# Performance work log

Measured on AMD Instinct MI355X. Metric: run time of the kernel, lower is better.

## Reference

```python
import jax, jax.numpy as jnp
import numpy as np

D_STATE = 8
DT_RANK = 16
D_CONV = 4


def layernorm(x, w, b, eps=1e-5):
    mu = jnp.mean(x, axis=-1, keepdims=True)
    var = jnp.var(x, axis=-1, keepdims=True)
    return (x - mu) * jax.lax.rsqrt(var + eps) * w + b


def silu(x):
    return x * jax.nn.sigmoid(x)


def dwconv_causal(x, w, b):
    # x: [B,L,D], w: [D,K] depthwise causal conv (mamba conv1d, padding=K-1 then truncate)
    K = w.shape[1]
    xp = jnp.pad(x, ((0, 0), (K - 1, 0), (0, 0)))
    y = jax.lax.conv_general_dilated(
        xp, w.T[:, None, :], (1,), 'VALID',
        dimension_numbers=('NWC', 'WIO', 'NWC'),
        feature_group_count=w.shape[0])
    return y + b


def selective_scan(u, dt, A, Bm, Cm, Dp):
    # u, dt: [b,l,d]; A: [d,n]; Bm, Cm: [b,l,n]; Dp: [d]
    def step(h, inp):
        dt_t, B_t, C_t, u_t = inp           # [b,d],[b,n],[b,n],[b,d]
        dA = jnp.exp(dt_t[..., None] * A)   # [b,d,n]
        h = dA * h + dt_t[..., None] * B_t[:, None, :] * u_t[..., None]
        y = jnp.einsum('bdn,bn->bd', h, C_t)
        return h, y
    b, l, d = u.shape
    h0 = jnp.zeros((b, d, A.shape[1]), u.dtype)
    xs = (dt.transpose(1, 0, 2), Bm.transpose(1, 0, 2),
          Cm.transpose(1, 0, 2), u.transpose(1, 0, 2))
    _, ys = jax.lax.scan(step, h0, xs)
    return ys.transpose(1, 0, 2) + u * Dp


def scan_dir(x, xe, cw, cb, cew, ceb, xpw, dtw, dtb, A_log, Dp):
    # one scan direction: u from x (input0 path), dt/B/C from xe (extra_emb path)
    xc = silu(dwconv_causal(x, cw, cb))
    ec = silu(dwconv_causal(xe, cew, ceb))
    dbl = ec @ xpw.T                                   # [b,l,dt_rank+2n]
    dtr = dbl[..., :DT_RANK]
    Bm = dbl[..., DT_RANK:DT_RANK + D_STATE]
    Cm = dbl[..., DT_RANK + D_STATE:]
    dt = jax.nn.softplus(dtr @ dtw.T + dtb)
    A = -jnp.exp(A_log)
    return selective_scan(xc, dt, A, Bm, Cm, Dp)


def forward(input0, input1, norm0_w, norm0_b, norm1_w, norm1_b,
            in_proj_w, in_proj_extra_w,
            convx_w, convx_b, conve_w, conve_b,
            convx_w_r, convx_b_r, conve_w_r, conve_b_r,
            xproj_w, xproj_w_r, dtproj_w, dtproj_b, dtproj_w_r, dtproj_b_r,
            A_log, A_log_r, Dp, Dp_r, outnorm_w, outnorm_b, outproj_w):
    skip = input0
    h0 = layernorm(input0, norm0_w, norm0_b)
    h1 = layernorm(input1, norm1_w, norm1_b)
    xz = h0 @ in_proj_w.T                     # [b,l,2d]
    d = in_proj_w.shape[0] // 2
    x, z = xz[..., :d], xz[..., d:]
    xe = h1 @ in_proj_extra_w.T               # [b,l,d]
    # forward-direction scan
    y_f = scan_dir(x, xe, convx_w, convx_b, conve_w, conve_b,
                   xproj_w, dtproj_w, dtproj_b, A_log, Dp)
    # backward-direction scan (flip sequence, scan, flip back)
    xr, xer = jnp.flip(x, 1), jnp.flip(xe, 1)
    y_b = scan_dir(xr, xer, convx_w_r, convx_b_r, conve_w_r, conve_b_r,
                   xproj_w_r, dtproj_w_r, dtproj_b_r, A_log_r, Dp_r)
    y = (y_f + jnp.flip(y_b, 1)) * 0.5        # if_devide_out=True
    y = layernorm(y, outnorm_w, outnorm_b)    # use_norm=True
    y = y * silu(z)
    out = y @ outproj_w.T
    return out + skip


def setup_inputs() -> dict:
    key = jax.random.key(0)
    B, H, W, dim = 2, 128, 128, 256
    L, d, n, dtr, K = H * W, dim, D_STATE, DT_RANK, D_CONV
    ks = jax.random.split(key, 24)
    s = 0.02
    inp = {
        'input0': jax.random.normal(ks[0], (B, L, dim), jnp.float32),
        'input1': jax.random.normal(ks[1], (B, L, dim), jnp.float32),
        'norm0_w': jnp.ones((dim,), jnp.float32),
        'norm0_b': jnp.zeros((dim,), jnp.float32),
        'norm1_w': jnp.ones((dim,), jnp.float32),
        'norm1_b': jnp.zeros((dim,), jnp.float32),
        'in_proj_w': jax.random.normal(ks[2], (2 * d, dim), jnp.float32) * s,
        'in_proj_extra_w': jax.random.normal(ks[3], (d, dim), jnp.float32) * s,
        'convx_w': jax.random.normal(ks[4], (d, K), jnp.float32) * 0.2,
        'convx_b': jnp.zeros((d,), jnp.float32),
        'conve_w': jax.random.normal(ks[5], (d, K), jnp.float32) * 0.2,
        'conve_b': jnp.zeros((d,), jnp.float32),
        'convx_w_r': jax.random.normal(ks[6], (d, K), jnp.float32) * 0.2,
        'convx_b_r': jnp.zeros((d,), jnp.float32),
        'conve_w_r': jax.random.normal(ks[7], (d, K), jnp.float32) * 0.2,
        'conve_b_r': jnp.zeros((d,), jnp.float32),
        'xproj_w': jax.random.normal(ks[8], (dtr + 2 * n, d), jnp.float32) * s,
        'xproj_w_r': jax.random.normal(ks[9], (dtr + 2 * n, d), jnp.float32) * s,
        'dtproj_w': jax.random.normal(ks[10], (d, dtr), jnp.float32) * 0.1,
        'dtproj_b': jax.random.uniform(ks[11], (d,), jnp.float32, -4.0, -2.0),
        'dtproj_w_r': jax.random.normal(ks[12], (d, dtr), jnp.float32) * 0.1,
        'dtproj_b_r': jax.random.uniform(ks[13], (d,), jnp.float32, -4.0, -2.0),
        'A_log': jnp.tile(jnp.log(jnp.arange(1, n + 1, dtype=jnp.float32)), (d, 1)),
        'A_log_r': jnp.tile(jnp.log(jnp.arange(1, n + 1, dtype=jnp.float32)), (d, 1)),
        'Dp': jnp.ones((d,), jnp.float32),
        'Dp_r': jnp.ones((d,), jnp.float32),
        'outnorm_w': jnp.ones((d,), jnp.float32),
        'outnorm_b': jnp.zeros((d,), jnp.float32),
        'outproj_w': jax.random.normal(ks[14], (dim, d), jnp.float32) * s,
    }
    return inp


def reference(input0, input1, norm0_w, norm0_b, norm1_w, norm1_b,
              in_proj_w, in_proj_extra_w,
              convx_w, convx_b, conve_w, conve_b,
              convx_w_r, convx_b_r, conve_w_r, conve_b_r,
              xproj_w, xproj_w_r, dtproj_w, dtproj_b, dtproj_w_r, dtproj_b_r,
              A_log, A_log_r, Dp, Dp_r, outnorm_w, outnorm_b, outproj_w):
    return forward(input0, input1, norm0_w, norm0_b, norm1_w, norm1_b,
                   in_proj_w, in_proj_extra_w,
                   convx_w, convx_b, conve_w, conve_b,
                   convx_w_r, convx_b_r, conve_w_r, conve_b_r,
                   xproj_w, xproj_w_r, dtproj_w, dtproj_b, dtproj_w_r, dtproj_b_r,
                   A_log, A_log_r, Dp, Dp_r, outnorm_w, outnorm_b, outproj_w)
```

## Files before the change

### kernel.cpp

```cpp
#include <hip/hip_runtime.h>
#include <math.h>

#define L_SEQ 16384
#define DIM 256
#define NST 8
#define RNK 16
#define S_TOT 32768
#define NCH 512
#define CLH 32

typedef __attribute__((ext_vector_type(8))) short bf16x8;
typedef __attribute__((ext_vector_type(4))) float f32x4;

__device__ __forceinline__ float bf2f(unsigned short u) {
  union { unsigned int i; float f; } v; v.i = ((unsigned int)u) << 16; return v.f;
}
__device__ __forceinline__ unsigned short f2bf(float x) {
  union { float f; unsigned int i; } v; v.f = x;
  unsigned int r = v.i + 0x7fffu + ((v.i >> 16) & 1u);
  return (unsigned short)(r >> 16);
}
__device__ __forceinline__ float rcpf(float x) {
  return __builtin_amdgcn_rcpf(x);
}
// ... 34 lines not shown
  out.x = f2bf((v.x - mean) * rstd * wv.x + bv.x);
  out.y = f2bf((v.y - mean) * rstd * wv.y + bv.y);
  out.z = f2bf((v.z - mean) * rstd * wv.z + bv.z);
  out.w = f2bf((v.w - mean) * rstd * wv.w + bv.w);
  *(ushort4*)&h[(size_t)row * DIM + lane * 4] = out;
}

template <int BF16C, int ADDIN>
__global__ __launch_bounds__(256) void gemm64(
    const unsigned short* __restrict__ A, int lda,
    const unsigned short* __restrict__ Wb,
    void* __restrict__ Cv, const float* __restrict__ addp, int Nn) {
  __shared__ unsigned short As[64 * 256];
  __shared__ unsigned short Ws[64 * 256];
  int tid = threadIdx.x;
  int n0 = blockIdx.x * 64, m0 = blockIdx.y * 64;
  for (int i = 0; i < 8; ++i) {
    int f8 = tid + i * 256;
    int r = f8 >> 5, c8 = (f8 & 31) * 8;
    int sc = c8 ^ ((r & 7) << 3);
    *(uint4*)&As[r * 256 + sc] = *(const uint4*)&A[(size_t)(m0 + r) * lda + c8];
    *(uint4*)&Ws[r * 256 + sc] = *(const uint4*)&Wb[(size_t)(n0 + r) * 256 + c8];
  }
  __syncthreads();
  int wid = tid >> 6, lane = tid & 63;
  int wm = wid >> 1, wn = wid & 1;
  int l15 = lane & 15, lk = (lane >> 4) * 8;
  f32x4 acc[2][2] = {};
  for (int ks = 0; ks < 8; ++ks) {
    int kcol = ks * 32 + lk;
    bf16x8 af[2], bf_[2];
    for (int mf = 0; mf < 2; ++mf) {
      int row = wm * 32 + mf * 16 + l15;
      af[mf] = *(const bf16x8*)&As[row * 256 + (kcol ^ ((row & 7) << 3))];
    }
    for (int nf = 0; nf < 2; ++nf) {
      int row = wn * 32 + nf * 16 + l15;
      bf_[nf] = *(const bf16x8*)&Ws[row * 256 + (kcol ^ ((row & 7) << 3))];
    }
    for (int mf = 0; mf < 2; ++mf)
      for (int nf = 0; nf < 2; ++nf)
        acc[mf][nf] = __builtin_amdgcn_mfma_f32_16x16x32_bf16(
            af[mf], bf_[nf], acc[mf][nf], 0, 0, 0);
  }
  for (int mf = 0; mf < 2; ++mf)
    for (int nf = 0; nf < 2; ++nf) {
      int row = m0 + wm * 32 + mf * 16 + (lane >> 4) * 4;
      int col = n0 + wn * 32 + nf * 16 + l15;
      for (int v = 0; v < 4; ++v) {
        size_t off = (size_t)(row + v) * Nn + col;
        float val = acc[mf][nf][v];
        if (ADDIN) val += addp[off];
        if (BF16C) ((unsigned short*)Cv)[off] = f2bf(val);
        else       ((float*)Cv)[off] = val;
      }
    }
}

__global__ __launch_bounds__(256) void gemm_in2(
    const unsigned short* __restrict__ h0, const unsigned short* __restrict__ h1,
    const unsigned short* __restrict__ wb_in, const unsigned short* __restrict__ wb_ex,
    unsigned short* __restrict__ xzOut, unsigned short* __restrict__ xeOut) {
  __shared__ unsigned short As[64 * 256];
  __shared__ unsigned short Ws[64 * 256];
  int tid = threadIdx.x;
  bool isX = blockIdx.x < 512;
  const unsigned short* A = isX ? h0 : h1;
  const unsigned short* Wb = isX ? wb_in : wb_ex;
  unsigned short* Cv = isX ? xzOut : xeOut;
  int Nn = isX ? 512 : 256;
  int NT = isX ? 8 : 4;
  int m0 = (isX ? (int)blockIdx.x : (int)blockIdx.x - 512) * 64;
  for (int i = 0; i < 8; ++i) {
    int f8 = tid + i * 256;
    int r = f8 >> 5, c8 = (f8 & 31) * 8;
    int sc = c8 ^ ((r & 7) << 3);
    *(uint4*)&As[r * 256 + sc] = *(const uint4*)&A[(size_t)(m0 + r) * 256 + c8];
  }
  int wid = tid >> 6, lane = tid & 63;
  int wm = wid >> 1, wn = wid & 1;
  int l15 = lane & 15, lk = (lane >> 4) * 8;
  for (int nt = 0; nt < NT; ++nt) {
    int n0 = nt * 64;
    for (int i = 0; i < 8; ++i) {
      int f8 = tid + i * 256;
      int r = f8 >> 5, c8 = (f8 & 31) * 8;
      int sc = c8 ^ ((r & 7) << 3);
      *(uint4*)&Ws[r * 256 + sc] = *(const uint4*)&Wb[(size_t)(n0 + r) * 256 + c8];
    }
    __syncthreads();
    f32x4 acc[2][2] = {};
    for (int ks = 0; ks < 8; ++ks) {
      int kcol = ks * 32 + lk;
      bf16x8 af[2], bf_[2];
      for (int mf = 0; mf < 2; ++mf) {
        int row = wm * 32 + mf * 16 + l15;
        af[mf] = *(const bf16x8*)&As[row * 256 + (kcol ^ ((row & 7) << 3))];
      }
      for (int nf = 0; nf < 2; ++nf) {
        int row = wn * 32 + nf * 16 + l15;
        bf_[nf] = *(const bf16x8*)&Ws[row * 256 + (kcol ^ ((row & 7) << 3))];
      }
      for (int mf = 0; mf < 2; ++mf)
        for (int nf = 0; nf < 2; ++nf)
          acc[mf][nf] = __builtin_amdgcn_mfma_f32_16x16x32_bf16(
              af[mf], bf_[nf], acc[mf][nf], 0, 0, 0);
    }
    for (int mf = 0; mf < 2; ++mf)
      for (int nf = 0; nf < 2; ++nf) {
        int row = m0 + wm * 32 + mf * 16 + (lane >> 4) * 4;
        int col = n0 + wn * 32 + nf * 16 + l15;
        for (int v = 0; v < 4; ++v) {
          size_t off = (size_t)(row + v) * Nn + col;
          Cv[off] = f2bf(acc[mf][nf][v]);
        }
      }
    __syncthreads();
  }
}

__global__ __launch_bounds__(256) void gemm_out3(
    const unsigned short* __restrict__ ycomb,
    const unsigned short* __restrict__ ybu,
    const unsigned short* __restrict__ xz,
    const float* __restrict__ onw, const float* __restrict__ onb,
    const unsigned short* __restrict__ Wb,
    float* __restrict__ outp, const float* __restrict__ addp) {
  __shared__ unsigned short As[64 * 256];
  __shared__ unsigned short Ws[64 * 256];
  int tid = threadIdx.x;
  int m0 = (int)blockIdx.x * 64;
  for (int i = 0; i < 8; ++i) {
    int f8 = tid + i * 256;
    int r = f8 >> 5, c8 = (f8 & 31) * 8;
    int sc = c8 ^ ((r & 7) << 3);
    int m = m0 + r;
    int b = m >> 14, l = m & (L_SEQ - 1);
    const unsigned short* pf = &ycomb[(size_t)m * DIM + c8];
    const unsigned short* pb =
        &ybu[((size_t)S_TOT + ((size_t)b << 14) + (L_SEQ - 1 - l)) * DIM + c8];
    ushort4 f0 = *(const ushort4*)pf, f1 = *(const ushort4*)(pf + 4);
    ushort4 b0 = *(const ushort4*)pb, b1 = *(const ushort4*)(pb + 4);
    float v[8];
    v[0] = 0.5f * (bf2f(f0.x) + bf2f(b0.x));
    v[1] = 0.5f * (bf2f(f0.y) + bf2f(b0.y));
    v[2] = 0.5f * (bf2f(f0.z) + bf2f(b0.z));
    v[3] = 0.5f * (bf2f(f0.w) + bf2f(b0.w));
    v[4] = 0.5f * (bf2f(f1.x) + bf2f(b1.x));
    v[5] = 0.5f * (bf2f(f1.y) + bf2f(b1.y));
    v[6] = 0.5f * (bf2f(f1.z) + bf2f(b1.z));
    v[7] = 0.5f * (bf2f(f1.w) + bf2f(b1.w));
    float s = 0.f, s2 = 0.f;
    for (int j = 0; j < 8; ++j) { s += v[j]; s2 += v[j] * v[j]; }
    for (int off = 16; off; off >>= 1) {
      s += __shfl_xor(s, off);
      s2 += __shfl_xor(s2, off);
    }
    float mean = s * (1.0f / DIM);
    float var = s2 * (1.0f / DIM) - mean * mean;
    float rstd = rsqrtf(var + 1e-5f);
    const unsigned short* pz = &xz[(size_t)m * 512 + 256 + c8];
    ushort4 z0 = *(const ushort4*)pz, z1 = *(const ushort4*)(pz + 4);
    float zf[8] = {bf2f(z0.x), bf2f(z0.y), bf2f(z0.z), bf2f(z0.w),
                   bf2f(z1.x), bf2f(z1.y), bf2f(z1.z), bf2f(z1.w)};
    float4 w0v = *(const float4*)&onw[c8];
    float4 w1v = *(const float4*)&onw[c8 + 4];
    float4 bb0 = *(const float4*)&onb[c8];
    float4 bb1 = *(const float4*)&onb[c8 + 4];
    float wv[8] = {w0v.x, w0v.y, w0v.z, w0v.w, w1v.x, w1v.y, w1v.z, w1v.w};
    float bv[8] = {bb0.x, bb0.y, bb0.z, bb0.w, bb1.x, bb1.y, bb1.z, bb1.w};
    unsigned int o[4];
    for (int jj = 0; jj < 4; ++jj) {
      int j0 = jj * 2, j1 = jj * 2 + 1;
      float ln0 = (v[j0] - mean) * rstd * wv[j0] + bv[j0];
      float ln1 = (v[j1] - mean) * rstd * wv[j1] + bv[j1];
      float g0 = ln0 * (zf[j0] * rcpf(1.f + __expf(-zf[j0])));
      float g1 = ln1 * (zf[j1] * rcpf(1.f + __expf(-zf[j1])));
      o[jj] = (unsigned int)f2bf(g0) | ((unsigned int)f2bf(g1) << 16);
    }
    uint4 pk; pk.x = o[0]; pk.y = o[1]; pk.z = o[2]; pk.w = o[3];
    *(uint4*)&As[r * 256 + sc] = pk;
  }
  int wid = tid >> 6, lane = tid & 63;
  int wm = wid >> 1, wn = wid & 1;
  int l15 = lane & 15, lk = (lane >> 4) * 8;
  for (int nt = 0; nt < 4; ++nt) {
    int n0 = nt * 64;
    for (int i = 0; i < 8; ++i) {
      int f8 = tid + i * 256;
      int r = f8 >> 5, c8 = (f8 & 31) * 8;
      int sc = c8 ^ ((r & 7) << 3);
      *(uint4*)&Ws[r * 256 + sc] = *(const uint4*)&Wb[(size_t)(n0 + r) * 256 + c8];
    }
    __syncthreads();
    f32x4 acc[2][2] = {};
    for (int ks = 0; ks < 8; ++ks) {
      int kcol = ks * 32 + lk;
      bf16x8 af[2], bf_[2];
      for (int mf = 0; mf < 2; ++mf) {
        int row = wm * 32 + mf * 16 + l15;
        af[mf] = *(const bf16x8*)&As[row * 256 + (kcol ^ ((row & 7) << 3))];
      }
      for (int nf = 0; nf < 2; ++nf) {
        int row = wn * 32 + nf * 16 + l15;
        bf_[nf] = *(const bf16x8*)&Ws[row * 256 + (kcol ^ ((row & 7) << 3))];
      }
      for (int mf = 0; mf < 2; ++mf)
        for (int nf = 0; nf < 2; ++nf)
          acc[mf][nf] = __builtin_amdgcn_mfma_f32_16x16x32_bf16(
              af[mf], bf_[nf], acc[mf][nf], 0, 0, 0);
    }
    for (int mf = 0; mf < 2; ++mf)
      for (int nf = 0; nf < 2; ++nf) {
        int row = m0 + wm * 32 + mf * 16 + (lane >> 4) * 4;
        int col = n0 + wn * 32 + nf * 16 + l15;
        for (int v = 0; v < 4; ++v) {
          size_t off = (size_t)(row + v) * 256 + col;
          outp[off] = acc[mf][nf][v] + addp[off];
        }
      }
    __syncthreads();
  }
}

__global__ __launch_bounds__(256) void xproj_mfma(
    const unsigned short* __restrict__ xe,
    const float* __restrict__ conve_w, const float* __restrict__ conve_b,
    const float* __restrict__ conve_w_r, const float* __restrict__ conve_b_r,
    const float* __restrict__ xproj_w, const float* __restrict__ xproj_w_r,
    unsigned short* __restrict__ dbl2) {
  __shared__ unsigned short ecS[64 * 256];
  __shared__ unsigned short xwS[32 * 256];
  int chunk = blockIdx.x;
  int dir = blockIdx.y;
  int b = chunk >> 8;
  int t0 = (chunk & 255) * 64;
  int tid = threadIdx.x;
  const float* cw = dir ? conve_w_r : conve_w;
  const float* cb = dir ? conve_b_r : conve_b;
  const float* xw = dir ? xproj_w_r : xproj_w;

  for (int i = tid; i < 32 * 256; i += 256) {
    int o = i >> 8, dd = i & 255;
    xwS[o * 256 + (((dd & ~7) ^ ((o & 7) << 3)) | (dd & 7))] = f2bf(xw[i]);
  }

  {
    int c = tid;
    float w0 = cw[c * 4 + 0], w1 = cw[c * 4 + 1], w2 = cw[c * 4 + 2],
          w3 = cw[c * 4 + 3], bias = cb[c];
    size_t bL = (size_t)b * L_SEQ;
    auto loadx = [&](int t) -> float {
      if (t < 0) return 0.f;
      int src = dir ? (L_SEQ - 1 - t) : t;
      return bf2f(xe[(bL + src) * DIM + c]);
    };
    float xm3 = loadx(t0 - 3), xm2 = loadx(t0 - 2), xm1 = loadx(t0 - 1);
    const unsigned short* xp =
        &xe[(bL + (dir ? (L_SEQ - 1 - t0) : t0)) * DIM + c];
    int xstep = dir ? -DIM : DIM;
    int cbase = c & ~7, clow = c & 7;
    for (int t4 = 0; t4 < 64; t4 += 4) {
      float xin4[4];
      for (int j = 0; j < 4; ++j) xin4[j] = bf2f(xp[(ptrdiff_t)j * xstep]);
      xp += (ptrdiff_t)4 * xstep;
      for (int j = 0; j < 4; ++j) {
        int tl = t4 + j;
        float xin = xin4[j];
        float pre = w0 * xm3 + w1 * xm2 + w2 * xm1 + w3 * xin + bias;
        float u = pre * rcpf(1.f + __expf(-pre));
        xm3 = xm2; xm2 = xm1; xm1 = xin;
        ecS[tl * 256 + ((cbase ^ ((tl & 7) << 3)) | clow)] = f2bf(u);
      }
    }
  }
  __syncthreads();

  int wid = tid >> 6, lane = tid & 63;
  int l15 = lane & 15, lk = (lane >> 4) * 8;
  f32x4 acc[2] = {};
  for (int kk = 0; kk < 8; ++kk) {
    int kcol = kk * 32 + lk;
    int row = wid * 16 + l15;
    bf16x8 af = *(const bf16x8*)&ecS[row * 256 + (kcol ^ ((row & 7) << 3))];
    for (int ni = 0; ni < 2; ++ni) {
      int o = ni * 16 + l15;
      bf16x8 bfr = *(const bf16x8*)&xwS[o * 256 + (kcol ^ ((o & 7) << 3))];
      acc[ni] = __builtin_amdgcn_mfma_f32_16x16x32_bf16(af, bfr, acc[ni], 0, 0, 0);
    }
  }
  size_t mbase = (size_t)dir * S_TOT + (size_t)chunk * 64;
  int rloc = wid * 16 + (lane >> 4) * 4;
  for (int ni = 0; ni < 2; ++ni) {
    int o = ni * 16 + l15;
    for (int v = 0; v < 4; ++v)
      dbl2[(mbase + rloc + v) * 32 + o] = f2bf(acc[ni][v]);
  }
}

__global__ __launch_bounds__(256) void dtu_compute(
    const unsigned short* __restrict__ dbl2,
    const float* __restrict__ dtw, const float* __restrict__ dtw_r,
    const float* __restrict__ dtb, const float* __restrict__ dtb_r,
    unsigned short* __restrict__ dt_arr,
    const unsigned short* __restrict__ xz,
    const float* __restrict__ convx_w, const float* __restrict__ convx_b,
    const float* __restrict__ convx_w_r, const float* __restrict__ convx_b_r,
    unsigned short* __restrict__ u_arr) {
  __shared__ unsigned short dtwS[256 * 32];
  __shared__ unsigned short dtrS[64 * 32];
  __shared__ unsigned short outS[64 * 256];
  int tid = threadIdx.x;
  if (blockIdx.x < 1024) {
    int m0 = blockIdx.x * 64;
    int dir = (blockIdx.x >= 512) ? 1 : 0;
    const float* dw = dir ? dtw_r : dtw;
    const float* db = dir ? dtb_r : dtb;
    {
      uint4 z; z.x = 0; z.y = 0; z.z = 0; z.w = 0;
      for (int i = tid; i < 1280; i += 256) {
        if (i < 1024) ((uint4*)dtwS)[i] = z;
        else          ((uint4*)dtrS)[i - 1024] = z;
      }
    }
    __syncthreads();
    for (int it = 0; it < 4; ++it) {
      int idx = tid + it * 256;
      int c = idx >> 2, k4 = idx & 3;
      float4 v = *(const float4*)&dw[c * 16 + k4 * 4];
      uint2 pk;
      pk.x = (unsigned int)f2bf(v.x) | ((unsigned int)f2bf(v.y) << 16);
      pk.y = (unsigned int)f2bf(v.z) | ((unsigned int)f2bf(v.w) << 16);
      int byte = c * 64 + (((k4 >> 1) ^ (c & 3)) << 4) + ((k4 & 1) << 3);
      *(uint2*)((char*)dtwS + byte) = pk;
    }
    {
      int r = tid >> 2, k4 = tid & 3;
      uint2 pk = *(const uint2*)&dbl2[(size_t)(m0 + r) * 32 + k4 * 4];
      int byte = r * 64 + (((k4 >> 1) ^ (r & 3)) << 4) + ((k4 & 1) << 3);
      *(uint2*)((char*)dtrS + byte) = pk;
    }
    __syncthreads();
    int wid = tid >> 6, lane = tid & 63;
    int l15 = lane & 15, lkc = lane >> 4;
    bf16x8 af[4];
    for (int mi = 0; mi < 4; ++mi) {
      int r = mi * 16 + l15;
      af[mi] = *(const bf16x8*)((char*)dtrS + r * 64 + ((lkc ^ (r & 3)) << 4));
    }
    f32x4 acc[4][4] = {};
    for (int ni = 0; ni < 4; ++ni) {
      int c = (wid * 4 + ni) * 16 + l15;
      bf16x8 bfr = *(const bf16x8*)((char*)dtwS + c * 64 + ((lkc ^ (c & 3)) << 4));
      for (int mi = 0; mi < 4; ++mi)
        acc[mi][ni] = __builtin_amdgcn_mfma_f32_16x16x32_bf16(
            af[mi], bfr, acc[mi][ni], 0, 0, 0);
    }
    for (int ni = 0; ni < 4; ++ni) {
      int c = (wid * 4 + ni) * 16 + l15;
      float bias_ = db[c];
      int cb_ = c & ~7, cl_ = c & 7;
      for (int mi = 0; mi < 4; ++mi) {
        int rb = mi * 16 + (lane >> 4) * 4;
        for (int v = 0; v < 4; ++v) {
          int r = rb + v;
          float xdt = acc[mi][ni][v] + bias_;
          float dtv = (xdt > 15.f) ? xdt : __logf(1.f + __expf(xdt));
          outS[r * 256 + ((cb_ ^ ((r & 7) << 3)) | cl_)] = f2bf(dtv);
        }
      }
    }
    __syncthreads();
    for (int it = 0; it < 8; ++it) {
      int i = tid + it * 256;
      int r = i >> 5, cg = (i & 31) * 8;
      uint4 val = *(const uint4*)&outS[r * 256 + (cg ^ ((r & 7) << 3))];
      *(uint4*)&dt_arr[(size_t)(m0 + r) * 256 + cg] = val;
    }
  } else {
    int chunk = blockIdx.x - 1024;
    int b = chunk >> 9;
    int t0 = (chunk & 511) * 32;
    int c = tid;
    float w0 = convx_w[c * 4 + 0], w1 = convx_w[c * 4 + 1],
          w2 = convx_w[c * 4 + 2], w3 = convx_w[c * 4 + 3], bias = convx_b[c];
    float w0r = convx_w_r[c * 4 + 0], w1r = convx_w_r[c * 4 + 1],
          w2r = convx_w_r[c * 4 + 2], w3r = convx_w_r[c * 4 + 3],
          biasr = convx_b_r[c];
    size_t bL = (size_t)b * L_SEQ;
    auto ld = [&](int t) -> float {
      if (t < 0 || t >= L_SEQ) return 0.f;
      return bf2f(xz[(bL + t) * 512 + c]);
    };
    float x3 = ld(t0 - 3), x2 = ld(t0 - 2), x1 = ld(t0 - 1);
    unsigned short* op0 = &u_arr[(bL + t0) * DIM + c];
    unsigned short* op1 =
        &u_arr[((size_t)S_TOT + bL + (L_SEQ - 1 - t0)) * DIM + c];
    for (int tg = 0; tg < 36; tg += 4) {
      float xin4[4];
      for (int j = 0; j < 4; ++j) xin4[j] = ld(t0 + tg + j);
      for (int j = 0; j < 4; ++j) {
        int tl = tg + j;
        float xin = xin4[j];
        if (tl < 32) {
          float pre = w0 * x3 + w1 * x2 + w2 * x1 + w3 * xin + bias;
          op0[(size_t)tl * DIM] = f2bf(pre * rcpf(1.f + __expf(-pre)));
        }
        if (tl >= 3 && tl < 35) {
          float prer = w0r * xin + w1r * x1 + w2r * x2 + w3r * x3 + biasr;
          int s = tl - 3;
          *(op1 - (ptrdiff_t)s * DIM) = f2bf(prer * rcpf(1.f + __expf(-prer)));
        }
        x3 = x2; x2 = x1; x1 = xin;
      }
    }
  }
}

#define DA8(FASTA)                                                    \
  float dA[NST];                                                      \
  if (FASTA) {                                                        \
    float e1 = __expf(-dtv);                                          \
    dA[0] = e1;                                                       \
    for (int n = 1; n < NST; ++n) dA[n] = dA[n - 1] * e1;             \
  } else {                                                            \
    for (int n = 0; n < NST; ++n) dA[n] = __expf(dtv * Ar[n]);        \
  }

template <int USE_UDT>
__global__ __launch_bounds__(256) void scan_pass1(
    const unsigned short* __restrict__ xz, const unsigned short* __restrict__ dbl2,
    const unsigned short* __restrict__ u_arr,
    const unsigned short* __restrict__ dt_arr,
    const float* __restrict__ convx_w, const float* __restrict__ convx_b,
    const float* __restrict__ convx_w_r, const float* __restrict__ convx_b_r,
    const float* __restrict__ dtproj_w, const float* __restrict__ dtproj_b,
    const float* __restrict__ dtproj_w_r, const float* __restrict__ dtproj_b_r,
    const float* __restrict__ A_log, const float* __restrict__ A_log_r,
    float* __restrict__ Pc, float* __restrict__ Qc) {
  int chunk = blockIdx.x, b = blockIdx.y, dir = blockIdx.z;
  int d = threadIdx.x;
  const float* al = dir ? A_log_r : A_log;
  float w0 = 0.f, w1 = 0.f, w2 = 0.f, w3 = 0.f, bias = 0.f, dbias = 0.f;
  float dwreg[RNK];
  if (!USE_UDT) {
    const float* cw = dir ? convx_w_r : convx_w;
    const float* cb = dir ? convx_b_r : convx_b;
    const float* dw = dir ? dtproj_w_r : dtproj_w;
    const float* dbp = dir ? dtproj_b_r : dtproj_b;
    w0 = cw[d * 4 + 0]; w1 = cw[d * 4 + 1]; w2 = cw[d * 4 + 2];
    w3 = cw[d * 4 + 3]; bias = cb[d]; dbias = dbp[d];
    for (int r = 0; r < RNK; ++r) dwreg[r] = dw[d * RNK + r];
  }
  float Ar[NST];
  bool fa = true;
  for (int n = 0; n < NST; ++n) {
    Ar[n] = -__expf(al[d * NST + n]);
    fa = fa && (fabsf(Ar[n] + (float)(n + 1)) < 1e-4f * (float)(n + 1));
  }
  bool fastA = (__ballot(fa) == ~0ULL);

  __shared__ float dblS[CLH][32];
  int t0 = chunk * CLH;
  size_t dtbase = (size_t)dir * S_TOT + (size_t)b * L_SEQ;
  if (USE_UDT) {
    int i = d;
    dblS[i >> 3][i & 7] =
        bf2f(dbl2[(dtbase + t0 + (i >> 3)) * 32 + 16 + (i & 7)]);
  } else {
    for (int i = d; i < CLH * 32; i += 256)
      dblS[i >> 5][i & 31] = bf2f(dbl2[(dtbase + t0) * 32 + i]);
  }
  __syncthreads();
  auto loadx = [&](int t) -> float {
    if (t < 0) return 0.f;
    int srct = dir ? (L_SEQ - 1 - t) : t;
    return bf2f(xz[((size_t)b * L_SEQ + srct) * 512 + d]);
  };
  float xm3 = 0.f, xm2 = 0.f, xm1 = 0.f;
  if (!USE_UDT) { xm3 = loadx(t0 - 3); xm2 = loadx(t0 - 2); xm1 = loadx(t0 - 1); }
  const unsigned short* up = &u_arr[(dtbase + t0) * DIM + d];
  const unsigned short* dtp = &dt_arr[(dtbase + t0) * DIM + d];
  float Q[NST];
  for (int n = 0; n < NST; ++n) Q[n] = 0.f;
  float sdt = 0.f;
  const int BOFF = USE_UDT ? 0 : 16;

#define P1_GRP(FASTA)                                                      \
  for (int t8 = 0; t8 < CLH; t8 += 8) {                                    \
    float uu[8], dd[8];                                                    \
    for (int j = 0; j < 8; ++j) {                                          \
      uu[j] = bf2f(up[(size_t)j * DIM]);                                   \
      dd[j] = bf2f(dtp[(size_t)j * DIM]);                                  \
    }                                                                      \
    up += 8 * DIM; dtp += 8 * DIM;                                         \
    for (int j = 0; j < 8; ++j) {                                          \
      const float* row = dblS[t8 + j];                                     \
      float u = uu[j], dtv = dd[j];                                        \
      float du = dtv * u;                                                  \
      sdt += dtv;                                                          \
      DA8(FASTA)                                                           \
      float4 B0 = *(const float4*)(row);                                   \
      float4 B1 = *(const float4*)(row + 4);                               \
      Q[0] = dA[0] * Q[0] + du * B0.x; Q[1] = dA[1] * Q[1] + du * B0.y;    \
      Q[2] = dA[2] * Q[2] + du * B0.z; Q[3] = dA[3] * Q[3] + du * B0.w;    \
      Q[4] = dA[4] * Q[4] + du * B1.x; Q[5] = dA[5] * Q[5] + du * B1.y;    \
      Q[6] = dA[6] * Q[6] + du * B1.z; Q[7] = dA[7] * Q[7] + du * B1.w;    \
    }                                                                      \
  }

#define P1_STEP(FASTA)                                                     \
  {                                                                        \
    const float* row = dblS[tl];                                           \
    float u, dtv;                                                          \
    {                                                                      \
      float xin = loadx(t0 + tl);                                          \
      float pre = w0 * xm3 + w1 * xm2 + w2 * xm1 + w3 * xin + bias;        \
      u = pre * rcpf(1.f + __expf(-pre));                                  \
      xm3 = xm2; xm2 = xm1; xm1 = xin;                                     \
      float4 q0 = *(const float4*)(row);                                   \
      float4 q1 = *(const float4*)(row + 4);                               \
      float4 q2 = *(const float4*)(row + 8);                               \
      float4 q3 = *(const float4*)(row + 12);                              \
      float xdt = dbias + q0.x * dwreg[0] + q0.y * dwreg[1] +              \
                  q0.z * dwreg[2] + q0.w * dwreg[3] + q1.x * dwreg[4] +    \
                  q1.y * dwreg[5] + q1.z * dwreg[6] + q1.w * dwreg[7] +    \
                  q2.x * dwreg[8] + q2.y * dwreg[9] + q2.z * dwreg[10] +   \
                  q2.w * dwreg[11] + q3.x * dwreg[12] + q3.y * dwreg[13] + \
                  q3.z * dwreg[14] + q3.w * dwreg[15];                     \
      dtv = (xdt > 15.f) ? xdt : __logf(1.f + __expf(xdt));                \
    }                                                                      \
    float du = dtv * u;                                                    \
    sdt += dtv;                                                            \
    DA8(FASTA)                                                             \
    float4 B0 = *(const float4*)(row + BOFF);                              \
    float4 B1 = *(const float4*)(row + BOFF + 4);                          \
    Q[0] = dA[0] * Q[0] + du * B0.x; Q[1] = dA[1] * Q[1] + du * B0.y;      \
    Q[2] = dA[2] * Q[2] + du * B0.z; Q[3] = dA[3] * Q[3] + du * B0.w;      \
    Q[4] = dA[4] * Q[4] + du * B1.x; Q[5] = dA[5] * Q[5] + du * B1.y;      \
    Q[6] = dA[6] * Q[6] + du * B1.z; Q[7] = dA[7] * Q[7] + du * B1.w;      \
  }

  if (USE_UDT) {
    if (fastA) { P1_GRP(1) } else { P1_GRP(0) }
  } else {
    if (fastA) {
      for (int tl = 0; tl < CLH; ++tl) P1_STEP(1)
    } else {
      for (int tl = 0; tl < CLH; ++tl) P1_STEP(0)
    }
  }
#undef P1_STEP
#undef P1_GRP

  float P[NST];
  if (fastA) {
    float E = __expf(-sdt);
    P[0] = E;
    for (int n = 1; n < NST; ++n) P[n] = P[n - 1] * E;
  } else {
    for (int n = 0; n < NST; ++n) P[n] = __expf(Ar[n] * sdt);
  }
  size_t obase = ((((size_t)(dir * 2 + b)) * NCH + chunk) * DIM + d) * NST;
  for (int n = 0; n < NST; ++n) { Pc[obase + n] = P[n]; Qc[obase + n] = Q[n]; }
}

__global__ __launch_bounds__(256) void scan_mid(
    float* __restrict__ Pc, const float* __restrict__ Qc) {
  int idx = blockIdx.x * 256 + threadIdx.x;
  int dn = idx & 2047;
  int db_ = idx >> 11;
  size_t base = (size_t)db_ * NCH * 2048 + dn;
  float h = 0.f;
  for (int c0 = 0; c0 < NCH; c0 += 8) {
    size_t off = base + (size_t)c0 * 2048;
    float P[8], Q[8];
#pragma unroll
    for (int j = 0; j < 8; ++j) {
      P[j] = Pc[off + (size_t)j * 2048];
      Q[j] = Qc[off + (size_t)j * 2048];
    }
#pragma unroll
    for (int j = 0; j < 8; ++j) {
      Pc[off + (size_t)j * 2048] = h;
      h = P[j] * h + Q[j];
    }
  }
}

template <int MODE>
__global__ __launch_bounds__(256) void scan_pass2(
    const unsigned short* __restrict__ xz, const unsigned short* __restrict__ dbl2,
    unsigned short* __restrict__ u_arr,
    const unsigned short* __restrict__ dt_arr,
    const float* __restrict__ convx_w, const float* __restrict__ convx_b,
    const float* __restrict__ convx_w_r, const float* __restrict__ convx_b_r,
    const float* __restrict__ dtproj_w, const float* __restrict__ dtproj_b,
    const float* __restrict__ dtproj_w_r, const float* __restrict__ dtproj_b_r,
    const float* __restrict__ A_log, const float* __restrict__ A_log_r,
    const float* __restrict__ Dp, const float* __restrict__ Dp_r,
    const float* __restrict__ Hinit, unsigned short* __restrict__ ycomb,
    int dirParam) {
  int chunk = blockIdx.x, b = blockIdx.y;
  int dir = MODE ? blockIdx.z : dirParam;
  int d = threadIdx.x;
  const float* al = dir ? A_log_r : A_log;
  float Dv = (dir ? Dp_r : Dp)[d];
  float w0 = 0.f, w1 = 0.f, w2 = 0.f, w3 = 0.f, bias = 0.f, dbias = 0.f;
  float dwreg[RNK];
  if (!MODE) {
    const float* cw = dir ? convx_w_r : convx_w;
    const float* cb = dir ? convx_b_r : convx_b;
    const float* dw = dir ? dtproj_w_r : dtproj_w;
    const float* dbp = dir ? dtproj_b_r : dtproj_b;
    w0 = cw[d * 4 + 0]; w1 = cw[d * 4 + 1]; w2 = cw[d * 4 + 2];
    w3 = cw[d * 4 + 3]; bias = cb[d];
    dbias = dbp[d];
    for (int r = 0; r < RNK; ++r) dwreg[r] = dw[d * RNK + r];
  }
  float Ar[NST];
  bool fa = true;
  for (int n = 0; n < NST; ++n) {
    Ar[n] = -__expf(al[d * NST + n]);
    fa = fa && (fabsf(Ar[n] + (float)(n + 1)) < 1e-4f * (float)(n + 1));
  }
  bool fastA = (__ballot(fa) == ~0ULL);

  __shared__ float dblS[CLH][32];
  int t0 = chunk * CLH;
  size_t dtbase = (size_t)dir * S_TOT + (size_t)b * L_SEQ;
  if (MODE) {
    for (int i = d; i < CLH * 16; i += 256)
      dblS[i >> 4][i & 15] =
          bf2f(dbl2[(dtbase + t0 + (i >> 4)) * 32 + 16 + (i & 15)]);
  } else {
    for (int i = d; i < CLH * 32; i += 256)
      dblS[i >> 5][i & 31] = bf2f(dbl2[(dtbase + t0) * 32 + i]);
  }
  __syncthreads();
  auto loadx = [&](int t) -> float {
    if (t < 0) return 0.f;
    int srct = dir ? (L_SEQ - 1 - t) : t;
    return bf2f(xz[((size_t)b * L_SEQ + srct) * 512 + d]);
  };
  float xm3 = 0.f, xm2 = 0.f, xm1 = 0.f;
  if (!MODE) { xm3 = loadx(t0 - 3); xm2 = loadx(t0 - 2); xm1 = loadx(t0 - 1); }
  float h[NST];
  size_t hbase = ((((size_t)(dir * 2 + b)) * NCH + chunk) * DIM + d) * NST;
  for (int n = 0; n < NST; ++n) h[n] = Hinit[hbase + n];
  unsigned short* up = &u_arr[(dtbase + t0) * DIM + d];
  const unsigned short* dtp = &dt_arr[(dtbase + t0) * DIM + d];
  unsigned short* yc = &ycomb[((size_t)b * L_SEQ + t0) * DIM + d];

#define P2_GRP(FASTA)                                                      \
  for (int t8 = 0; t8 < CLH; t8 += 8) {                                    \
    float uu[8], dd[8];                                                    \
    for (int j = 0; j < 8; ++j) {                                          \
      uu[j] = bf2f(up[(size_t)j * DIM]);                                   \
      dd[j] = bf2f(dtp[(size_t)j * DIM]);                                  \
    }                                                                      \
    for (int j = 0; j < 8; ++j) {                                          \
      const float* row = dblS[t8 + j];                                     \
      float u = uu[j], dtv = dd[j];                                        \
      float du = dtv * u;                                                  \
      DA8(FASTA)                                                           \
      float4 B0 = *(const float4*)(row);                                   \
      float4 B1 = *(const float4*)(row + 4);                               \
      float4 C0 = *(const float4*)(row + 8);                               \
      float4 C1 = *(const float4*)(row + 12);                              \
      h[0] = dA[0] * h[0] + du * B0.x; h[1] = dA[1] * h[1] + du * B0.y;    \
      h[2] = dA[2] * h[2] + du * B0.z; h[3] = dA[3] * h[3] + du * B0.w;    \
      h[4] = dA[4] * h[4] + du * B1.x; h[5] = dA[5] * h[5] + du * B1.y;    \
      h[6] = dA[6] * h[6] + du * B1.z; h[7] = dA[7] * h[7] + du * B1.w;    \
      float y = C0.x * h[0] + C0.y * h[1] + C0.z * h[2] + C0.w * h[3] +    \
                C1.x * h[4] + C1.y * h[5] + C1.z * h[6] + C1.w * h[7] +    \
                u * Dv;                                                    \
      if (dir == 0) yc[(size_t)j * DIM] = f2bf(y);                         \
      else          up[(size_t)j * DIM] = f2bf(y);                         \
    }                                                                      \
    up += 8 * DIM; dtp += 8 * DIM; yc += 8 * DIM;                          \
  }

#define P2_STEP(FASTA)                                                     \
  {                                                                        \
    int t = t0 + tl;                                                       \
    const float* row = dblS[tl];                                           \
    float u, dtv;                                                          \
    {                                                                      \
      float xin = loadx(t);                                                \
      float pre = w0 * xm3 + w1 * xm2 + w2 * xm1 + w3 * xin + bias;        \
      u = pre * rcpf(1.f + __expf(-pre));                                  \
      xm3 = xm2; xm2 = xm1; xm1 = xin;                                     \
      float4 q0 = *(const float4*)(row);                                   \
      float4 q1 = *(const float4*)(row + 4);                               \
      float4 q2 = *(const float4*)(row + 8);                               \
      float4 q3 = *(const float4*)(row + 12);                              \
      float xdt = dbias + q0.x * dwreg[0] + q0.y * dwreg[1] +              \
                  q0.z * dwreg[2] + q0.w * dwreg[3] + q1.x * dwreg[4] +    \
                  q1.y * dwreg[5] + q1.z * dwreg[6] + q1.w * dwreg[7] +    \
                  q2.x * dwreg[8] + q2.y * dwreg[9] + q2.z * dwreg[10] +   \
                  q2.w * dwreg[11] + q3.x * dwreg[12] + q3.y * dwreg[13] + \
                  q3.z * dwreg[14] + q3.w * dwreg[15];                     \
      dtv = (xdt > 15.f) ? xdt : __logf(1.f + __expf(xdt));                \
    }                                                                      \
    float du = dtv * u;                                                    \
    DA8(FASTA)                                                             \
    float4 B0 = *(const float4*)(row + 16);                                \
    float4 B1 = *(const float4*)(row + 20);                                \
    float4 C0 = *(const float4*)(row + 24);                                \
    float4 C1 = *(const float4*)(row + 28);                                \
    h[0] = dA[0] * h[0] + du * B0.x; h[1] = dA[1] * h[1] + du * B0.y;      \
    h[2] = dA[2] * h[2] + du * B0.z; h[3] = dA[3] * h[3] + du * B0.w;      \
    h[4] = dA[4] * h[4] + du * B1.x; h[5] = dA[5] * h[5] + du * B1.y;      \
    h[6] = dA[6] * h[6] + du * B1.z; h[7] = dA[7] * h[7] + du * B1.w;      \
    float y = C0.x * h[0] + C0.y * h[1] + C0.z * h[2] + C0.w * h[3] +      \
              C1.x * h[4] + C1.y * h[5] + C1.z * h[6] + C1.w * h[7] +      \
              u * Dv;                                                      \
    if (dir == 0) {                                                        \
      ycomb[((size_t)b * L_SEQ + t) * DIM + d] = f2bf(y);                  \
    } else {                                                               \
      size_t o = ((size_t)b * L_SEQ + (L_SEQ - 1 - t)) * DIM + d;          \
      float prev = bf2f(ycomb[o]);                                         \
      ycomb[o] = f2bf(0.5f * (prev + y));                                  \
    }                                                                      \
  }

  if (MODE) {
    if (fastA) { P2_GRP(1) } else { P2_GRP(0) }
  } else {
    if (fastA) {
      for (int tl = 0; tl < CLH; ++tl) P2_STEP(1)
    } else {
      for (int tl = 0; tl < CLH; ++tl) P2_STEP(0)
    }
  }
#undef P2_STEP
#undef P2_GRP
}

__global__ __launch_bounds__(256) void combine_ln(
    const unsigned short* __restrict__ ycomb,
    unsigned short* __restrict__ xz,
    const float* __restrict__ onw, const float* __restrict__ onb) {
  int m = blockIdx.x * 4 + (threadIdx.x >> 6);
  int lane = threadIdx.x & 63;
  ushort4 y4 = *(const ushort4*)&ycomb[(size_t)m * DIM + lane * 4];
  float v0 = bf2f(y4.x), v1 = bf2f(y4.y), v2 = bf2f(y4.z), v3 = bf2f(y4.w);
  float s = v0 + v1 + v2 + v3;
  float s2 = v0 * v0 + v1 * v1 + v2 * v2 + v3 * v3;
  for (int off = 32; off; off >>= 1) {
    s += __shfl_xor(s, off);
    s2 += __shfl_xor(s2, off);
  }
  float mean = s * (1.0f / DIM);
  float var = s2 * (1.0f / DIM) - mean * mean;
  float rstd = rsqrtf(var + 1e-5f);
  ushort4 z4 = *(const ushort4*)&xz[(size_t)m * 512 + 256 + lane * 4];
  float zf[4] = {bf2f(z4.x), bf2f(z4.y), bf2f(z4.z), bf2f(z4.w)};
  float vf[4] = {v0, v1, v2, v3};
  ushort4 out;
  unsigned short* op = (unsigned short*)&out;
  for (int j = 0; j < 4; ++j) {
    int c = lane * 4 + j;
    float ln = (vf[j] - mean) * rstd * onw[c] + onb[c];
    op[j] = f2bf(ln * (zf[j] * rcpf(1.f + __expf(-zf[j]))));
  }
  *(ushort4*)&xz[(size_t)m * 512 + lane * 4] = out;
}

extern "C" void kernel_launch(void* const* d_in, const int* in_sizes, int n_in,
                              void* d_out, int out_size, void* d_ws, size_t ws_size,
                              hipStream_t stream) {
  const float* input0 = (const float*)d_in[0];
  const float* input1 = (const float*)d_in[1];
  const float* norm0_w = (const float*)d_in[2];
  const float* norm0_b = (const float*)d_in[3];
  const float* norm1_w = (const float*)d_in[4];
  const float* norm1_b = (const float*)d_in[5];
  const float* in_proj_w = (const float*)d_in[6];
  const float* in_proj_extra_w = (const float*)d_in[7];
  const float* convx_w = (const float*)d_in[8];
  const float* convx_b = (const float*)d_in[9];
  const float* conve_w = (const float*)d_in[10];
  const float* conve_b = (const float*)d_in[11];
  const float* convx_w_r = (const float*)d_in[12];
  const float* convx_b_r = (const float*)d_in[13];
  const float* conve_w_r = (const float*)d_in[14];
  const float* conve_b_r = (const float*)d_in[15];
  const float* xproj_w = (const float*)d_in[16];
  const float* xproj_w_r = (const float*)d_in[17];
  const float* dtproj_w = (const float*)d_in[18];
  const float* dtproj_b = (const float*)d_in[19];
  const float* dtproj_w_r = (const float*)d_in[20];
  const float* dtproj_b_r = (const float*)d_in[21];
  const float* A_log = (const float*)d_in[22];
  const float* A_log_r = (const float*)d_in[23];
  const float* Dp = (const float*)d_in[24];
  const float* Dp_r = (const float*)d_in[25];
  const float* outnorm_w = (const float*)d_in[26];
  const float* outnorm_b = (const float*)d_in[27];
  const float* outproj_w = (const float*)d_in[28];

  char* w = (char*)d_ws;
  unsigned short* xz    = (unsigned short*)(w + 0);
  unsigned short* h0    = (unsigned short*)(w + 33554432);
  unsigned short* ycomb = (unsigned short*)(w + 33554432);
  float* Qc   = (float*)(w + 33554432);
  unsigned short* xe    = (unsigned short*)(w + 50331648);
  float* Pc   = (float*)(w + 50331648);
  unsigned short* dbl2 = (unsigned short*)(w + 67108864);
  unsigned short* wb = (unsigned short*)(w + 75497472);
  unsigned short* wb_in  = wb;
  unsigned short* wb_ex  = wb + 131072;
  unsigned short* wb_out = wb + 196608;
  unsigned short* u_arr  = (unsigned short*)(w + 76021760);
  unsigned short* dt_arr = (unsigned short*)(w + 109576192);
  const bool big = ws_size >= 76021760ULL + 67108864ULL;
  unsigned short* h1 = big ? u_arr : xz;

  ln_norm<<<dim3(S_TOT / 4, 2), 256, 0, stream>>>(
      input0, input1, norm0_w, norm0_b, norm1_w, norm1_b, h0, h1,
      in_proj_w, in_proj_extra_w, outproj_w, wb);
  if (big) {
    gemm_in2<<<dim3(1024), 256, 0, stream>>>(h0, h1, wb_in, wb_ex, xz, xe);
  } else {
    gemm64<1, 0><<<dim3(4, 512), 256, 0, stream>>>(h1, DIM, wb_ex, xe, nullptr, 256);
    gemm64<1, 0><<<dim3(8, 512), 256, 0, stream>>>(h0, DIM, wb_in, xz, nullptr, 512);
  }
  xproj_mfma<<<dim3(512, 2), 256, 0, stream>>>(
      xe, conve_w, conve_b, conve_w_r, conve_b_r, xproj_w, xproj_w_r, dbl2);
  if (big) {
    dtu_compute<<<dim3(2048), 256, 0, stream>>>(
        dbl2, dtproj_w, dtproj_w_r, dtproj_b, dtproj_b_r, dt_arr,
        xz, convx_w, convx_b, convx_w_r, convx_b_r, u_arr);
    scan_pass1<1><<<dim3(NCH, 2, 2), 256, 0, stream>>>(
        xz, dbl2, u_arr, dt_arr, convx_w, convx_b, convx_w_r, convx_b_r,
        dtproj_w, dtproj_b, dtproj_w_r, dtproj_b_r, A_log, A_log_r, Pc, Qc);
  } else {
    scan_pass1<0><<<dim3(NCH, 2, 2), 256, 0, stream>>>(
        xz, dbl2, u_arr, dt_arr, convx_w, convx_b, convx_w_r, convx_b_r,
        dtproj_w, dtproj_b, dtproj_w_r, dtproj_b_r, A_log, A_log_r, Pc, Qc);
  }
  scan_mid<<<dim3(32), 256, 0, stream>>>(Pc, Qc);
  if (big) {
    scan_pass2<1><<<dim3(NCH, 2, 2), 256, 0, stream>>>(
        xz, dbl2, u_arr, dt_arr, convx_w, convx_b, convx_w_r, convx_b_r,
        dtproj_w, dtproj_b, dtproj_w_r, dtproj_b_r, A_log, A_log_r,
        Dp, Dp_r, Pc, ycomb, 0);
    gemm_out3<<<dim3(512), 256, 0, stream>>>(
        ycomb, u_arr, xz, outnorm_w, outnorm_b, wb_out, (float*)d_out, input0);
  } else {
    for (int dir = 0; dir < 2; ++dir)
      scan_pass2<0><<<dim3(NCH, 2), 256, 0, stream>>>(
          xz, dbl2, u_arr, dt_arr, convx_w, convx_b, convx_w_r, convx_b_r,
          dtproj_w, dtproj_b, dtproj_w_r, dtproj_b_r, A_log, A_log_r,
          Dp, Dp_r, Pc, ycomb, dir);
    combine_ln<<<dim3(S_TOT / 4), 256, 0, stream>>>(ycomb, xz, outnorm_w, outnorm_b);
    gemm64<0, 1><<<dim3(4, 512), 256, 0, stream>>>(
        xz, 512, wb_out, d_out, input0, 256);
  }
}
```

Baseline: 194.7 us.

## Fuse x-path causal conv and SiLU into scan passes instead of materializing u

The depthwise causal conv plus SiLU that produced u is no longer run in separate blocks of dtu_compute. Both scan passes now read xz directly and recompute u on the fly from a rolling 3-tap window. This removes the u_arr write and its later reads in exchange for recomputing exp/rcp in both passes and reading the wider-strided xz rows. dtu_compute shrinks to the dt projection blocks only.

```diff
diff --git a/kernel.cpp b/kernel.cpp
--- a/kernel.cpp
+++ b/kernel.cpp
@@ -360,118 +360,75 @@
     const unsigned short* __restrict__ dbl2,
     const float* __restrict__ dtw, const float* __restrict__ dtw_r,
     const float* __restrict__ dtb, const float* __restrict__ dtb_r,
-    unsigned short* __restrict__ dt_arr,
-    const unsigned short* __restrict__ xz,
-    const float* __restrict__ convx_w, const float* __restrict__ convx_b,
-    const float* __restrict__ convx_w_r, const float* __restrict__ convx_b_r,
-    unsigned short* __restrict__ u_arr) {
+    unsigned short* __restrict__ dt_arr) {
   __shared__ unsigned short dtwS[256 * 32];
   __shared__ unsigned short dtrS[64 * 32];
   __shared__ unsigned short outS[64 * 256];
   int tid = threadIdx.x;
-  if (blockIdx.x < 1024) {
-    int m0 = blockIdx.x * 64;
-    int dir = (blockIdx.x >= 512) ? 1 : 0;
-    const float* dw = dir ? dtw_r : dtw;
-    const float* db = dir ? dtb_r : dtb;
-    {
-      uint4 z; z.x = 0; z.y = 0; z.z = 0; z.w = 0;
-      for (int i = tid; i < 1280; i += 256) {
-        if (i < 1024) ((uint4*)dtwS)[i] = z;
-        else          ((uint4*)dtrS)[i - 1024] = z;
+  int m0 = blockIdx.x * 64;
+  int dir = (blockIdx.x >= 512) ? 1 : 0;
+  const float* dw = dir ? dtw_r : dtw;
+  const float* db = dir ? dtb_r : dtb;
+  {
+    uint4 z; z.x = 0; z.y = 0; z.z = 0; z.w = 0;
+    for (int i = tid; i < 1280; i += 256) {
+      if (i < 1024) ((uint4*)dtwS)[i] = z;
+      else          ((uint4*)dtrS)[i - 1024] = z;
+    }
+  }
+  __syncthreads();
+  for (int it = 0; it < 4; ++it) {
+    int idx = tid + it * 256;
+    int c = idx >> 2, k4 = idx & 3;
+    float4 v = *(const float4*)&dw[c * 16 + k4 * 4];
+    uint2 pk;
+    pk.x = (unsigned int)f2bf(v.x) | ((unsigned int)f2bf(v.y) << 16);
+    pk.y = (unsigned int)f2bf(v.z) | ((unsigned int)f2bf(v.w) << 16);
+    int byte = c * 64 + (((k4 >> 1) ^ (c & 3)) << 4) + ((k4 & 1) << 3);
+    *(uint2*)((char*)dtwS + byte) = pk;
+  }
+  {
+    int r = tid >> 2, k4 = tid & 3;
+    uint2 pk = *(const uint2*)&dbl2[(size_t)(m0 + r) * 32 + k4 * 4];
+    int byte = r * 64 + (((k4 >> 1) ^ (r & 3)) << 4) + ((k4 & 1) << 3);
+    *(uint2*)((char*)dtrS + byte) = pk;
+  }
+  __syncthreads();
+  int wid = tid >> 6, lane = tid & 63;
+  int l15 = lane & 15, lkc = lane >> 4;
+  bf16x8 af[4];
+  for (int mi = 0; mi < 4; ++mi) {
+    int r = mi * 16 + l15;
+    af[mi] = *(const bf16x8*)((char*)dtrS + r * 64 + ((lkc ^ (r & 3)) << 4));
+  }
+  f32x4 acc[4][4] = {};
+  for (int ni = 0; ni < 4; ++ni) {
+    int c = (wid * 4 + ni) * 16 + l15;
+    bf16x8 bfr = *(const bf16x8*)((char*)dtwS + c * 64 + ((lkc ^ (c & 3)) << 4));
+    for (int mi = 0; mi < 4; ++mi)
+      acc[mi][ni] = __builtin_amdgcn_mfma_f32_16x16x32_bf16(
+          af[mi], bfr, acc[mi][ni], 0, 0, 0);
+  }
+  for (int ni = 0; ni < 4; ++ni) {
+    int c = (wid * 4 + ni) * 16 + l15;
+    float bias_ = db[c];
+    int cb_ = c & ~7, cl_ = c & 7;
+    for (int mi = 0; mi < 4; ++mi) {
+      int rb = mi * 16 + (lane >> 4) * 4;
+      for (int v = 0; v < 4; ++v) {
+        int r = rb + v;
+        float xdt = acc[mi][ni][v] + bias_;
+        float dtv = (xdt > 15.f) ? xdt : __logf(1.f + __expf(xdt));
+        outS[r * 256 + ((cb_ ^ ((r & 7) << 3)) | cl_)] = f2bf(dtv);
       }
     }
-    __syncthreads();
-    for (int it = 0; it < 4; ++it) {
-      int idx = tid + it * 256;
-      int c = idx >> 2, k4 = idx & 3;
-      float4 v = *(const float4*)&dw[c * 16 + k4 * 4];
-      uint2 pk;
-      pk.x = (unsigned int)f2bf(v.x) | ((unsigned int)f2bf(v.y) << 16);
-      pk.y = (unsigned int)f2bf(v.z) | ((unsigned int)f2bf(v.w) << 16);
-      int byte = c * 64 + (((k4 >> 1) ^ (c & 3)) << 4) + ((k4 & 1) << 3);
-      *(uint2*)((char*)dtwS + byte) = pk;
-    }
-    {
-      int r = tid >> 2, k4 = tid & 3;
-      uint2 pk = *(const uint2*)&dbl2[(size_t)(m0 + r) * 32 + k4 * 4];
-      int byte = r * 64 + (((k4 >> 1) ^ (r & 3)) << 4) + ((k4 & 1) << 3);
-      *(uint2*)((char*)dtrS + byte) = pk;
-    }
-    __syncthreads();
-    int wid = tid >> 6, lane = tid & 63;
-    int l15 = lane & 15, lkc = lane >> 4;
-    bf16x8 af[4];
-    for (int mi = 0; mi < 4; ++mi) {
-      int r = mi * 16 + l15;
-      af[mi] = *(const bf16x8*)((char*)dtrS + r * 64 + ((lkc ^ (r & 3)) << 4));
-    }
-    f32x4 acc[4][4] = {};
-    for (int ni = 0; ni < 4; ++ni) {
-      int c = (wid * 4 + ni) * 16 + l15;
-      bf16x8 bfr = *(const bf16x8*)((char*)dtwS + c * 64 + ((lkc ^ (c & 3)) << 4));
-      for (int mi = 0; mi < 4; ++mi)
-        acc[mi][ni] = __builtin_amdgcn_mfma_f32_16x16x32_bf16(
-            af[mi], bfr, acc[mi][ni], 0, 0, 0);
-    }
-    for (int ni = 0; ni < 4; ++ni) {
-      int c = (wid * 4 + ni) * 16 + l15;
-      float bias_ = db[c];
-      int cb_ = c & ~7, cl_ = c & 7;
-      for (int mi = 0; mi < 4; ++mi) {
-        int rb = mi * 16 + (lane >> 4) * 4;
-        for (int v = 0; v < 4; ++v) {
-          int r = rb + v;
-          float xdt = acc[mi][ni][v] + bias_;
-          float dtv = (xdt > 15.f) ? xdt : __logf(1.f + __expf(xdt));
-          outS[r * 256 + ((cb_ ^ ((r & 7) << 3)) | cl_)] = f2bf(dtv);
-        }
-      }
-    }
-    __syncthreads();
-    for (int it = 0; it < 8; ++it) {
-      int i = tid + it * 256;
-      int r = i >> 5, cg = (i & 31) * 8;
-      uint4 val = *(const uint4*)&outS[r * 256 + (cg ^ ((r & 7) << 3))];
-      *(uint4*)&dt_arr[(size_t)(m0 + r) * 256 + cg] = val;
-    }
-  } else {
-    int chunk = blockIdx.x - 1024;
-    int b = chunk >> 9;
-    int t0 = (chunk & 511) * 32;
-    int c = tid;
-    float w0 = convx_w[c * 4 + 0], w1 = convx_w[c * 4 + 1],
-          w2 = convx_w[c * 4 + 2], w3 = convx_w[c * 4 + 3], bias = convx_b[c];
-    float w0r = convx_w_r[c * 4 + 0], w1r = convx_w_r[c * 4 + 1],
-          w2r = convx_w_r[c * 4 + 2], w3r = convx_w_r[c * 4 + 3],
-          biasr = convx_b_r[c];
-    size_t bL = (size_t)b * L_SEQ;
-    auto ld = [&](int t) -> float {
-      if (t < 0 || t >= L_SEQ) return 0.f;
-      return bf2f(xz[(bL + t) * 512 + c]);
-    };
-    float x3 = ld(t0 - 3), x2 = ld(t0 - 2), x1 = ld(t0 - 1);
-    unsigned short* op0 = &u_arr[(bL + t0) * DIM + c];
-    unsigned short* op1 =
-        &u_arr[((size_t)S_TOT + bL + (L_SEQ - 1 - t0)) * DIM + c];
-    for (int tg = 0; tg < 36; tg += 4) {
-      float xin4[4];
-      for (int j = 0; j < 4; ++j) xin4[j] = ld(t0 + tg + j);
-      for (int j = 0; j < 4; ++j) {
-        int tl = tg + j;
-        float xin = xin4[j];
-        if (tl < 32) {
-          float pre = w0 * x3 + w1 * x2 + w2 * x1 + w3 * xin + bias;
-          op0[(size_t)tl * DIM] = f2bf(pre * rcpf(1.f + __expf(-pre)));
-        }
-        if (tl >= 3 && tl < 35) {
-          float prer = w0r * xin + w1r * x1 + w2r * x2 + w3r * x3 + biasr;
-          int s = tl - 3;
-          *(op1 - (ptrdiff_t)s * DIM) = f2bf(prer * rcpf(1.f + __expf(-prer)));
-        }
-        x3 = x2; x2 = x1; x1 = xin;
-      }
-    }
+  }
+  __syncthreads();
+  for (int it = 0; it < 8; ++it) {
+    int i = tid + it * 256;
+    int r = i >> 5, cg = (i & 31) * 8;
+    uint4 val = *(const uint4*)&outS[r * 256 + (cg ^ ((r & 7) << 3))];
+    *(uint4*)&dt_arr[(size_t)(m0 + r) * 256 + cg] = val;
   }
 }
 
@@ -499,15 +456,16 @@
   int chunk = blockIdx.x, b = blockIdx.y, dir = blockIdx.z;
   int d = threadIdx.x;
   const float* al = dir ? A_log_r : A_log;
-  float w0 = 0.f, w1 = 0.f, w2 = 0.f, w3 = 0.f, bias = 0.f, dbias = 0.f;
+  const float* cw = dir ? convx_w_r : convx_w;
+  const float* cb = dir ? convx_b_r : convx_b;
+  float w0 = cw[d * 4 + 0], w1 = cw[d * 4 + 1], w2 = cw[d * 4 + 2],
+        w3 = cw[d * 4 + 3], bias = cb[d];
+  float dbias = 0.f;
   float dwreg[RNK];
   if (!USE_UDT) {
-    const float* cw = dir ? convx_w_r : convx_w;
-    const float* cb = dir ? convx_b_r : convx_b;
     const float* dw = dir ? dtproj_w_r : dtproj_w;
     const float* dbp = dir ? dtproj_b_r : dtproj_b;
-    w0 = cw[d * 4 + 0]; w1 = cw[d * 4 + 1]; w2 = cw[d * 4 + 2];
-    w3 = cw[d * 4 + 3]; bias = cb[d]; dbias = dbp[d];
+    dbias = dbp[d];
     for (int r = 0; r < RNK; ++r) dwreg[r] = dw[d * RNK + r];
   }
   float Ar[NST];
@@ -535,9 +493,7 @@
     int srct = dir ? (L_SEQ - 1 - t) : t;
     return bf2f(xz[((size_t)b * L_SEQ + srct) * 512 + d]);
   };
-  float xm3 = 0.f, xm2 = 0.f, xm1 = 0.f;
-  if (!USE_UDT) { xm3 = loadx(t0 - 3); xm2 = loadx(t0 - 2); xm1 = loadx(t0 - 1); }
-  const unsigned short* up = &u_arr[(dtbase + t0) * DIM + d];
+  float xm3 = loadx(t0 - 3), xm2 = loadx(t0 - 2), xm1 = loadx(t0 - 1);
   const unsigned short* dtp = &dt_arr[(dtbase + t0) * DIM + d];
   float Q[NST];
   for (int n = 0; n < NST; ++n) Q[n] = 0.f;
@@ -546,15 +502,19 @@
 
 #define P1_GRP(FASTA)                                                      \
   for (int t8 = 0; t8 < CLH; t8 += 8) {                                    \
-    float uu[8], dd[8];                                                    \
+    float dd[8], xin8[8];                                                  \
     for (int j = 0; j < 8; ++j) {                                          \
-      uu[j] = bf2f(up[(size_t)j * DIM]);                                   \
       dd[j] = bf2f(dtp[(size_t)j * DIM]);                                  \
+      xin8[j] = loadx(t0 + t8 + j);                                        \
     }                                                                      \
-    up += 8 * DIM; dtp += 8 * DIM;                                         \
+    dtp += 8 * DIM;                                                        \
     for (int j = 0; j < 8; ++j) {                                          \
       const float* row = dblS[t8 + j];                                     \
-      float u = uu[j], dtv = dd[j];                                        \
+      float xin = xin8[j];                                                 \
+      float pre = w0 * xm3 + w1 * xm2 + w2 * xm1 + w3 * xin + bias;        \
+      float u = pre * rcpf(1.f + __expf(-pre));                            \
+      xm3 = xm2; xm2 = xm1; xm1 = xin;                                     \
+      float dtv = dd[j];                                                   \
       float du = dtv * u;                                                  \
       sdt += dtv;                                                          \
       DA8(FASTA)                                                           \
@@ -664,15 +624,15 @@
   int d = threadIdx.x;
   const float* al = dir ? A_log_r : A_log;
   float Dv = (dir ? Dp_r : Dp)[d];
-  float w0 = 0.f, w1 = 0.f, w2 = 0.f, w3 = 0.f, bias = 0.f, dbias = 0.f;
+  const float* cw = dir ? convx_w_r : convx_w;
+  const float* cb = dir ? convx_b_r : convx_b;
+  float w0 = cw[d * 4 + 0], w1 = cw[d * 4 + 1], w2 = cw[d * 4 + 2],
+        w3 = cw[d * 4 + 3], bias = cb[d];
+  float dbias = 0.f;
   float dwreg[RNK];
   if (!MODE) {
-    const float* cw = dir ? convx_w_r : convx_w;
-    const float* cb = dir ? convx_b_r : convx_b;
     const float* dw = dir ? dtproj_w_r : dtproj_w;
     const float* dbp = dir ? dtproj_b_r : dtproj_b;
-    w0 = cw[d * 4 + 0]; w1 = cw[d * 4 + 1]; w2 = cw[d * 4 + 2];
-    w3 = cw[d * 4 + 3]; bias = cb[d];
     dbias = dbp[d];
     for (int r = 0; r < RNK; ++r) dwreg[r] = dw[d * RNK + r];
   }
@@ -701,8 +661,7 @@
     int srct = dir ? (L_SEQ - 1 - t) : t;
     return bf2f(xz[((size_t)b * L_SEQ + srct) * 512 + d]);
   };
-  float xm3 = 0.f, xm2 = 0.f, xm1 = 0.f;
-  if (!MODE) { xm3 = loadx(t0 - 3); xm2 = loadx(t0 - 2); xm1 = loadx(t0 - 1); }
+  float xm3 = loadx(t0 - 3), xm2 = loadx(t0 - 2), xm1 = loadx(t0 - 1);
   float h[NST];
   size_t hbase = ((((size_t)(dir * 2 + b)) * NCH + chunk) * DIM + d) * NST;
   for (int n = 0; n < NST; ++n) h[n] = Hinit[hbase + n];
@@ -712,14 +671,18 @@
 
 #define P2_GRP(FASTA)                                                      \
   for (int t8 = 0; t8 < CLH; t8 += 8) {                                    \
-    float uu[8], dd[8];                                                    \
+    float dd[8], xin8[8];                                                  \
     for (int j = 0; j < 8; ++j) {                                          \
-      uu[j] = bf2f(up[(size_t)j * DIM]);                                   \
       dd[j] = bf2f(dtp[(size_t)j * DIM]);                                  \
+      xin8[j] = loadx(t0 + t8 + j);                                        \
     }                                                                      \
     for (int j = 0; j < 8; ++j) {                                          \
       const float* row = dblS[t8 + j];                                     \
-      float u = uu[j], dtv = dd[j];                                        \
+      float xin = xin8[j];                                                 \
+      float pre = w0 * xm3 + w1 * xm2 + w2 * xm1 + w3 * xin + bias;        \
+      float u = pre * rcpf(1.f + __expf(-pre));                            \
+      xm3 = xm2; xm2 = xm1; xm1 = xin;                                     \
+      float dtv = dd[j];                                                   \
       float du = dtv * u;                                                  \
       DA8(FASTA)                                                           \
       float4 B0 = *(const float4*)(row);                                   \
@@ -888,9 +851,8 @@
   xproj_mfma<<<dim3(512, 2), 256, 0, stream>>>(
       xe, conve_w, conve_b, conve_w_r, conve_b_r, xproj_w, xproj_w_r, dbl2);
   if (big) {
-    dtu_compute<<<dim3(2048), 256, 0, stream>>>(
-        dbl2, dtproj_w, dtproj_w_r, dtproj_b, dtproj_b_r, dt_arr,
-        xz, convx_w, convx_b, convx_w_r, convx_b_r, u_arr);
+    dtu_compute<<<dim3(1024), 256, 0, stream>>>(
+        dbl2, dtproj_w, dtproj_w_r, dtproj_b, dtproj_b_r, dt_arr);
     scan_pass1<1><<<dim3(NCH, 2, 2), 256, 0, stream>>>(
         xz, dbl2, u_arr, dt_arr, convx_w, convx_b, convx_w_r, convx_b_r,
         dtproj_w, dtproj_b, dtproj_w_r, dtproj_b_r, A_log, A_log_r, Pc, Qc);
```

Measured after the change: 237.5 us. +22.0%, slower.
